# Performance work log

Hardware: AMD Instinct MI355X
Metric: run time of the kernel (lower is better)

Reference implementation:

```python
import jax, jax.numpy as jnp
import numpy as np

DIM = 768
HEADS = 12
DIM_HEAD = DIM // HEADS
FACTOR = DIM_HEAD ** (-0.5)
B, T = 4, 2048


def setup_inputs() -> dict:
    key = jax.random.key(0)
    k1, k2, k3 = jax.random.split(key, 3)
    x = jax.random.normal(k1, (B, T, DIM), dtype=jnp.float32)
    # VarianceScaling-like init scale for linear weights
    W_qkv = jax.random.normal(k2, (DIM, 3 * DIM), dtype=jnp.float32) * (DIM ** -0.5)
    W_out = jax.random.normal(k3, (DIM, DIM), dtype=jnp.float32) * (DIM ** -0.5)
    return {"x": x, "W_qkv": W_qkv, "W_out": W_out}


def reference(x, W_qkv, W_out):
    b, t, _ = x.shape
    qkv = x @ W_qkv  # [b, t, 3*dim]
    # einops 'b t (d k h) -> k b h t d' with k=3, h=HEADS: d slowest, k middle, h fastest
    qkv = qkv.reshape(b, t, DIM_HEAD, 3, HEADS)
    qkv = jnp.transpose(qkv, (3, 0, 4, 1, 2))  # [3, b, h, t, d]
    q, k, v = qkv[0], qkv[1], qkv[2]
    # scaled dot-product attention, full [b,h,t,t] scores as in the original
    scores = jnp.einsum('bhid,bhjd->bhij', q, k) * FACTOR
    attn = jax.nn.softmax(scores, axis=-1)
    out = jnp.einsum('bhij,bhjd->bhid', attn, v)  # [b, h, t, d]
    # 'b h t d -> b t (h d)'
    out = jnp.transpose(out, (0, 2, 1, 3)).reshape(b, t, HEADS * DIM_HEAD)
    return out @ W_out
```

## Files before the change

### kernel.cpp

```cpp
#include <hip/hip_runtime.h>
#include <hip/hip_bf16.h>

#define DIM    768
#define HEADS  12
#define DHEAD  64
#define BATCH  4
#define SEQ    2048
#define NROW   (BATCH * SEQ)
#define QKVN   (3 * DIM)
#define FACTOR 0.125f
#define QSCALE 0.18033688011112042f

typedef __attribute__((ext_vector_type(8))) short short8;
typedef __attribute__((ext_vector_type(4))) float floatx4;

__device__ __forceinline__ floatx4 mfma16(short8 a, short8 b, floatx4 c) {
    return __builtin_amdgcn_mfma_f32_16x16x32_bf16(a, b, c, 0, 0, 0);
}

__device__ __forceinline__ void glds16(const void* g, void* l) {
    __builtin_amdgcn_global_load_lds((const __attribute__((address_space(1))) void*)g,
                                     (__attribute__((address_space(3))) void*)l,
                                     16, 0, 0);
}

__device__ __forceinline__ short rne16(float f) {
    unsigned u = __builtin_bit_cast(unsigned, f);
    return (short)((u + 0x7fffu + ((u >> 16) & 1u)) >> 16);
}
__device__ __forceinline__ unsigned pack2(float lo, float hi) {
    unsigned ul = __builtin_bit_cast(unsigned, lo);
    unsigned uh = __builtin_bit_cast(unsigned, hi);
    ul = (ul + 0x7fffu + ((ul >> 16) & 1u)) >> 16;
    uh = (uh + 0x7fffu + ((uh >> 16) & 1u)) & 0xffff0000u;
    return ul | uh;
}
__device__ __forceinline__ unsigned cvtpk(float lo, float hi) {
    unsigned r;
    asm("v_cvt_pk_bf16_f32 %0, %1, %2" : "=v"(r) : "v"(lo), "v"(hi));
    return r;
}

__device__ __forceinline__ int swz8(int row, int col) {
    return (row << 6) + ((((col >> 3) ^ row) & 7) << 3) + (col & 7);
}

__global__ __launch_bounds__(256) void prep(const float* __restrict__ x,
                                            short* __restrict__ xb,
                                            const float* __restrict__ Wqkv,
                                            short* __restrict__ Wqt,
                                            const float* __restrict__ Wout,
                                            short* __restrict__ Wot) {
    __shared__ short T[32][33];
    int blk = blockIdx.x;
    if (blk < 6144) {
        int g = blk * 256 + threadIdx.x;
        float4 v = ((const float4*)x)[g];
        uint2 o;
        o.x = pack2(v.x, v.y);
        o.y = pack2(v.z, v.w);
        ((uint2*)xb)[g] = o;
        return;
    }
    blk -= 6144;
    const float* W;
    short* Wt;
    int N, permute, bx, by;
    if (blk < 1728) { W = Wqkv; Wt = Wqt; N = QKVN; permute = 1; bx = blk % 72; by = blk / 72; }
    else { blk -= 1728; W = Wout; Wt = Wot; N = DIM; permute = 0; bx = blk % 24; by = blk / 24; }

    int n0 = bx * 32, k0 = by * 32;
    int c = threadIdx.x & 31, r0 = threadIdx.x >> 5;
    for (int r = r0; r < 32; r += 8)
        T[r][c] = rne16(W[(size_t)(k0 + r) * N + n0 + c]);
    __syncthreads();
    for (int r = r0; r < 32; r += 8) {
        int n = n0 + r;
        int np = n;
        float scale = 1.0f;
        if (permute) {
            int d = n / 36, rem = n - d * 36;
            int which = rem / 12, h = rem - which * 12;
            np = which * 768 + h * 64 + d;
            if (which == 0) scale = QSCALE;
        }
        float v = __bfloat162float(__hip_bfloat16_raw{(unsigned short)T[c][r]});
        Wt[(size_t)np * DIM + k0 + c] = (scale == 1.0f) ? T[c][r] : rne16(v * scale);
    }
}

__global__ __launch_bounds__(256) void gemm_qkv(const short* __restrict__ A,
                                                const short* __restrict__ Bt,
                                                short* __restrict__ Qo,
                                                short* __restrict__ Ko,
                                                short* __restrict__ Vto) {
    __shared__ short As[128 * 64];
    __shared__ short Bs[128 * 64];
    const int tid = threadIdx.x;
    const int lane = tid & 63, wave = tid >> 6;
    const int l15 = lane & 15, quad = lane >> 4;

    const int flat = blockIdx.x;
    const int xcd = flat & 7;
    const int local = flat >> 3;
    const int mloc = local & 7, nloc = local >> 3;
    const int m0 = (xcd * 8 + mloc) * 128;
    const int n0 = nloc * 128;

    const int wm = (wave >> 1) * 64, wn = (wave & 1) * 64;
    const int r8 = wave * 8 + (lane >> 3);
    const int c8 = lane & 7;
    const int sc = ((c8 ^ (r8 & 7)) << 3);

    const int sn = n0 + wn;
    const int which = sn / 768;
    const bool swapAB = (which != 2);

    floatx4 acc[4][4] = {};
    for (int k0 = 0; k0 < DIM; k0 += 64) {
#pragma unroll
        for (int i = 0; i < 4; ++i) {
            int row = i * 32 + r8;
            glds16(&A[(size_t)(m0 + row) * DIM + k0 + sc], &As[(size_t)(i * 32 + wave * 8) * 64]);
            glds16(&Bt[(size_t)(n0 + row) * DIM + k0 + sc], &Bs[(size_t)(i * 32 + wave * 8) * 64]);
        }
        __syncthreads();
#pragma unroll
        for (int ks = 0; ks < 2; ++ks) {
            short8 a[4], b[4];
#pragma unroll
            for (int mt = 0; mt < 4; ++mt)
                a[mt] = *(const short8*)&As[swz8(wm + mt * 16 + l15, ks * 32 + quad * 8)];
#pragma unroll
            for (int nt = 0; nt < 4; ++nt)
                b[nt] = *(const short8*)&Bs[swz8(wn + nt * 16 + l15, ks * 32 + quad * 8)];
            if (swapAB) {
#pragma unroll
                for (int mt = 0; mt < 4; ++mt)
#pragma unroll
                    for (int nt = 0; nt < 4; ++nt)
                        acc[mt][nt] = mfma16(b[nt], a[mt], acc[mt][nt]);
            } else {
#pragma unroll
                for (int mt = 0; mt < 4; ++mt)
#pragma unroll
                    for (int nt = 0; nt < 4; ++nt)
                        acc[mt][nt] = mfma16(a[mt], b[nt], acc[mt][nt]);
            }
        }
        __syncthreads();
    }

    const int h = (sn - which * 768) >> 6;
    const int bb = (m0 + wm) >> 11;
    const int tbase = (m0 + wm) & 2047;
    const size_t tilebase = ((size_t)(bb * HEADS + h) * 32 + (tbase >> 6)) * 4096;

    if (which != 2) {
        short* dst = (which == 0) ? Qo : Ko;
#pragma unroll
        for (int mt = 0; mt < 4; ++mt)
#pragma unroll
            for (int nt = 0; nt < 4; ++nt) {
                int tl = mt * 16 + l15;
                int d0 = nt * 16 + quad * 4;
                uint2 pk;
                pk.x = pack2(acc[mt][nt][0], acc[mt][nt][1]);
                pk.y = pack2(acc[mt][nt][2], acc[mt][nt][3]);
                *(uint2*)&dst[tilebase + swz8(tl, d0)] = pk;
            }
    } else {
        short* vld = ((wave < 2) ? As : Bs) + (wave & 1) * 4096;
#pragma unroll
        for (int mt = 0; mt < 4; ++mt)
#pragma unroll
            for (int nt = 0; nt < 4; ++nt) {
                int d = nt * 16 + l15;
                int tl = mt * 16 + quad * 4;
                int chunk = (tl >> 3) ^ (d & 7);
                int addr = (d << 6) + (chunk << 3) + (tl & 7);
                uint2 pk;
                pk.x = pack2(acc[mt][nt][0], acc[mt][nt][1]);
                pk.y = pack2(acc[mt][nt][2], acc[mt][nt][3]);
                *(uint2*)&vld[addr] = pk;
            }
    }
    __syncthreads();
    if (which == 2) {
        short* vld = ((wave < 2) ? As : Bs) + (wave & 1) * 4096;
#pragma unroll
        for (int i = 0; i < 8; ++i) {
            int c = (i * 64 + lane) * 8;
            *(uint4*)&Vto[tilebase + c] = *(const uint4*)&vld[c];
        }
    }
}

__global__ __launch_bounds__(512, 6) void attn_mfma(const short* __restrict__ Q,
                                                    const short* __restrict__ K,
                                                    const short* __restrict__ Vt,
                                                    short* __restrict__ O) {
    __shared__ __align__(16) short smem[24576];
    const int tid = threadIdx.x;
    const int lane = tid & 63, wave = tid >> 6;
    const int l15 = lane & 15, quad = lane >> 4;
    const int flat = blockIdx.x;
    const int xcd = flat & 7, li = flat >> 3;
    const int bh = xcd + (li % 6) * 8;
    const int q0 = (li / 6) * 128;
    const size_t base = (size_t)bh * SEQ * DHEAD;
    short* Pp = smem + 16384 + wave * 1024;
    const int lane8 = lane * 8;

    {
        size_t qtb = base + (size_t)(q0 >> 6) * 4096;
#pragma unroll
        for (int c = 0; c < 2; ++c) {
            int i = wave * 2 + c;
            glds16(&Q[qtb + (size_t)i * 512 + lane8], &smem[i * 512]);
        }
    }
    __syncthreads();
    short8 qf[2];
#pragma unroll
    for (int ks = 0; ks < 2; ++ks)
        qf[ks] = *(const short8*)&smem[(wave >> 2) * 4096 +
                                       swz8((wave & 3) * 16 + l15,
                                            ks * 32 + quad * 8)];
    __syncthreads();

    floatx4 o[4] = {};
    float lsum = 0.f;

    glds16(&K[base + wave * 512 + lane8], &smem[wave * 512]);
    glds16(&Vt[base + wave * 512 + lane8], &smem[4096 + wave * 512]);

    for (int t = 0; t < 32; ++t) {
        __syncthreads();
        short* Ks = smem + (t & 1) * 8192;
        short* Vs = Ks + 4096;
        if (t < 31) {
            size_t ktb = base + (size_t)(t + 1) * 4096;
            short* nb = smem + ((t + 1) & 1) * 8192;
            glds16(&K[ktb + wave * 512 + lane8], &nb[wave * 512]);
            glds16(&Vt[ktb + wave * 512 + lane8], &nb[4096 + wave * 512]);
        }

        floatx4 sa[4] = {};
        __builtin_amdgcn_s_setprio(1);
#pragma unroll
        for (int ks = 0; ks < 2; ++ks)
#pragma unroll
            for (int kt = 0; kt < 4; ++kt) {
                short8 kf = *(const short8*)&Ks[swz8(kt * 16 + l15, ks * 32 + quad * 8)];
                sa[kt] = mfma16(kf, qf[ks], sa[kt]);
            }
        __builtin_amdgcn_s_setprio(0);

#pragma unroll
        for (int kt = 0; kt < 4; ++kt) {
            float p0 = __builtin_amdgcn_exp2f(sa[kt][0]);
            float p1 = __builtin_amdgcn_exp2f(sa[kt][1]);
            float p2 = __builtin_amdgcn_exp2f(sa[kt][2]);
            float p3 = __builtin_amdgcn_exp2f(sa[kt][3]);
            lsum += (p0 + p1) + (p2 + p3);
            uint2 pk;
            pk.x = cvtpk(p0, p1);
            pk.y = cvtpk(p2, p3);
            *(uint2*)&Pp[swz8(l15, kt * 16 + quad * 4)] = pk;
        }

#pragma unroll
        for (int ks = 0; ks < 2; ++ks) {
            short8 pf = *(const short8*)&Pp[swz8(l15, ks * 32 + quad * 8)];
            __builtin_amdgcn_s_setprio(1);
#pragma unroll
            for (int dt = 0; dt < 4; ++dt) {
                short8 vf = *(const short8*)&Vs[swz8(dt * 16 + l15, ks * 32 + quad * 8)];
                o[dt] = mfma16(vf, pf, o[dt]);
            }
            __builtin_amdgcn_s_setprio(0);
        }
    }

    float s = lsum;
    s += __shfl_xor(s, 16);
    s += __shfl_xor(s, 32);
    float inv = 1.f / s;

    const int b = bh / HEADS, h = bh - b * HEADS;
    const int tq = q0 + wave * 16 + l15;
    size_t rowo = ((size_t)(b * SEQ + tq)) * DIM + h * DHEAD + quad * 4;
#pragma unroll
    for (int dt = 0; dt < 4; ++dt) {
        uint2 pk;
        pk.x = cvtpk(o[dt][0] * inv, o[dt][1] * inv);
        pk.y = cvtpk(o[dt][2] * inv, o[dt][3] * inv);
        *(uint2*)&O[rowo + dt * 16] = pk;
    }
}

__global__ __launch_bounds__(256) void gemm_out(const short* __restrict__ A,
                                                const short* __restrict__ Bt,
                                                float* __restrict__ out) {
    __shared__ short As[128 * 64];
    __shared__ short Bs[128 * 64];
    const int tid = threadIdx.x;
    const int lane = tid & 63, wave = tid >> 6;
    const int l15 = lane & 15, quad = lane >> 4;
    const int m0 = blockIdx.y * 128, n0 = blockIdx.x * 128;
    const int wm = (wave >> 1) * 64, wn = (wave & 1) * 64;
    const int r8 = wave * 8 + (lane >> 3);
    const int sc = (((lane & 7) ^ (r8 & 7)) << 3);

    floatx4 acc[4][4] = {};
    for (int k0 = 0; k0 < DIM; k0 += 64) {
#pragma unroll
        for (int i = 0; i < 4; ++i) {
            int row = i * 32 + r8;
            glds16(&A[(size_t)(m0 + row) * DIM + k0 + sc], &As[(size_t)(i * 32 + wave * 8) * 64]);
            glds16(&Bt[(size_t)(n0 + row) * DIM + k0 + sc], &Bs[(size_t)(i * 32 + wave * 8) * 64]);
        }
        __syncthreads();
#pragma unroll
        for (int ks = 0; ks < 2; ++ks) {
            short8 a[4], b[4];
#pragma unroll
            for (int mt = 0; mt < 4; ++mt)
                a[mt] = *(const short8*)&As[swz8(wm + mt * 16 + l15, ks * 32 + quad * 8)];
#pragma unroll
            for (int nt = 0; nt < 4; ++nt)
                b[nt] = *(const short8*)&Bs[swz8(wn + nt * 16 + l15, ks * 32 + quad * 8)];
#pragma unroll
            for (int mt = 0; mt < 4; ++mt)
#pragma unroll
                for (int nt = 0; nt < 4; ++nt)
                    acc[mt][nt] = mfma16(b[nt], a[mt], acc[mt][nt]);
        }
        __syncthreads();
    }

#pragma unroll
    for (int mt = 0; mt < 4; ++mt)
#pragma unroll
        for (int nt = 0; nt < 4; ++nt) {
            int m = m0 + wm + mt * 16 + l15;
            int n = n0 + wn + nt * 16 + quad * 4;
            *(floatx4*)&out[(size_t)m * DIM + n] = acc[mt][nt];
        }
}

extern "C" void kernel_launch(void* const* d_in, const int* in_sizes, int n_in,
                              void* d_out, int out_size, void* d_ws, size_t ws_size,
                              hipStream_t stream) {
    const float* x    = (const float*)d_in[0];
    const float* Wqkv = (const float*)d_in[1];
    const float* Wout = (const float*)d_in[2];
    float* out = (float*)d_out;

    const size_t NE = (size_t)NROW * DIM;
    short* xb  = (short*)d_ws;
    short* Wqt = xb + NE;
    short* Wot = Wqt + (size_t)QKVN * DIM;
    short* Qw  = Wot + (size_t)DIM * DIM;
    short* Kw  = Qw + NE;
    short* Vtw = Kw + NE;

    prep<<<6144 + 1728 + 576, 256, 0, stream>>>(x, xb, Wqkv, Wqt, Wout, Wot);
    gemm_qkv<<<8 * 8 * 18, 256, 0, stream>>>(xb, Wqt, Qw, Kw, Vtw);
    attn_mfma<<<768, 512, 0, stream>>>(Qw, Kw, Vtw, xb);
    gemm_out<<<dim3(DIM / 128, NROW / 128), 256, 0, stream>>>(xb, Wot, out);
}
```

Before: 210.1 us.

## Switch attention to 32x32x16 MFMA with register-only P via permlane swaps

Attention now uses 32x32x16 bf16 MFMA with 4 waves of 32 query rows each, instead of 8 waves of 16 rows using 16x16x32. The softmax probabilities are repacked into B-operand fragments in registers with v_permlane32_swap, which removes the LDS round-trip for P. The QKV GEMM epilogue writes Q, K and Vt directly in the fragment-native layout, dropping the LDS transpose and the extra barrier for V. This reduces LDS traffic and instruction count, at the cost of fewer waves per block and more registers per wave.

```diff
diff --git a/kernel.cpp b/kernel.cpp
--- a/kernel.cpp
+++ b/kernel.cpp
@@ -13,9 +13,14 @@
 
 typedef __attribute__((ext_vector_type(8))) short short8;
 typedef __attribute__((ext_vector_type(4))) float floatx4;
+typedef __attribute__((ext_vector_type(16))) float floatx16;
+typedef __attribute__((ext_vector_type(4))) unsigned uintx4;
 
 __device__ __forceinline__ floatx4 mfma16(short8 a, short8 b, floatx4 c) {
     return __builtin_amdgcn_mfma_f32_16x16x32_bf16(a, b, c, 0, 0, 0);
+}
+__device__ __forceinline__ floatx16 mfma32(short8 a, short8 b, floatx16 c) {
+    return __builtin_amdgcn_mfma_f32_32x32x16_bf16(a, b, c, 0, 0, 0);
 }
 
 __device__ __forceinline__ void glds16(const void* g, void* l) {
@@ -153,150 +158,168 @@
 
     const int h = (sn - which * 768) >> 6;
     const int bb = (m0 + wm) >> 11;
-    const int tbase = (m0 + wm) & 2047;
-    const size_t tilebase = ((size_t)(bb * HEADS + h) * 32 + (tbase >> 6)) * 4096;
 
     if (which != 2) {
-        short* dst = (which == 0) ? Qo : Ko;
+        const bool isQ = (which == 0);
+        short* dst = isQ ? Qo : Ko;
+        const size_t tb = isQ
+            ? ((size_t)(bb * HEADS + h) * 16 + ((m0 & 2047) >> 7)) * 8192
+            : ((size_t)(bb * HEADS + h) * 32 + (((m0 + wm) & 2047) >> 6)) * 4096;
 #pragma unroll
         for (int mt = 0; mt < 4; ++mt)
 #pragma unroll
             for (int nt = 0; nt < 4; ++nt) {
-                int tl = mt * 16 + l15;
-                int d0 = nt * 16 + quad * 4;
+                int cl = (mt & 1) * 16 + l15 + 32 * (quad >> 1);
+                int off = isQ
+                    ? (((wm >> 5) + (mt >> 1)) * 2048 + nt * 512 + cl * 8 + (quad & 1) * 4)
+                    : (((mt >> 1) * 4 + nt) * 512 + cl * 8 + (quad & 1) * 4);
                 uint2 pk;
                 pk.x = pack2(acc[mt][nt][0], acc[mt][nt][1]);
                 pk.y = pack2(acc[mt][nt][2], acc[mt][nt][3]);
-                *(uint2*)&dst[tilebase + swz8(tl, d0)] = pk;
+                *(uint2*)&dst[tb + off] = pk;
             }
     } else {
-        short* vld = ((wave < 2) ? As : Bs) + (wave & 1) * 4096;
+        const size_t tb = ((size_t)(bb * HEADS + h) * 32 + (((m0 + wm) & 2047) >> 6)) * 4096;
 #pragma unroll
         for (int mt = 0; mt < 4; ++mt)
 #pragma unroll
             for (int nt = 0; nt < 4; ++nt) {
-                int d = nt * 16 + l15;
-                int tl = mt * 16 + quad * 4;
-                int chunk = (tl >> 3) ^ (d & 7);
-                int addr = (d << 6) + (chunk << 3) + (tl & 7);
+                int cl = (nt & 1) * 16 + l15 + 32 * (quad >> 1);
+                int off = ((nt >> 1) * 4 + mt) * 512 + cl * 8 + (quad & 1) * 4;
                 uint2 pk;
                 pk.x = pack2(acc[mt][nt][0], acc[mt][nt][1]);
                 pk.y = pack2(acc[mt][nt][2], acc[mt][nt][3]);
-                *(uint2*)&vld[addr] = pk;
+                *(uint2*)&Vto[tb + off] = pk;
             }
     }
-    __syncthreads();
-    if (which == 2) {
-        short* vld = ((wave < 2) ? As : Bs) + (wave & 1) * 4096;
-#pragma unroll
-        for (int i = 0; i < 8; ++i) {
-            int c = (i * 64 + lane) * 8;
-            *(uint4*)&Vto[tilebase + c] = *(const uint4*)&vld[c];
-        }
-    }
-}
-
-__global__ __launch_bounds__(512, 6) void attn_mfma(const short* __restrict__ Q,
+}
+
+__global__ __launch_bounds__(256, 3) void attn_mfma(const short* __restrict__ Q,
                                                     const short* __restrict__ K,
                                                     const short* __restrict__ Vt,
                                                     short* __restrict__ O) {
-    __shared__ __align__(16) short smem[24576];
+    __shared__ __align__(16) short smem[16384];
     const int tid = threadIdx.x;
     const int lane = tid & 63, wave = tid >> 6;
-    const int l15 = lane & 15, quad = lane >> 4;
+    const int l31 = lane & 31, hi = lane >> 5;
     const int flat = blockIdx.x;
     const int xcd = flat & 7, li = flat >> 3;
     const int bh = xcd + (li % 6) * 8;
     const int q0 = (li / 6) * 128;
     const size_t base = (size_t)bh * SEQ * DHEAD;
-    short* Pp = smem + 16384 + wave * 1024;
     const int lane8 = lane * 8;
 
     {
-        size_t qtb = base + (size_t)(q0 >> 6) * 4096;
-#pragma unroll
-        for (int c = 0; c < 2; ++c) {
-            int i = wave * 2 + c;
-            glds16(&Q[qtb + (size_t)i * 512 + lane8], &smem[i * 512]);
+        size_t qtb = base + (size_t)(q0 >> 7) * 8192;
+#pragma unroll
+        for (int c = 0; c < 4; ++c) {
+            int s = wave * 4 + c;
+            glds16(&Q[qtb + s * 512 + lane8], &smem[s * 512]);
         }
     }
     __syncthreads();
-    short8 qf[2];
-#pragma unroll
-    for (int ks = 0; ks < 2; ++ks)
-        qf[ks] = *(const short8*)&smem[(wave >> 2) * 4096 +
-                                       swz8((wave & 3) * 16 + l15,
-                                            ks * 32 + quad * 8)];
+    short8 qf[4];
+#pragma unroll
+    for (int ks = 0; ks < 4; ++ks)
+        qf[ks] = *(const short8*)&smem[wave * 2048 + ks * 512 + lane8];
     __syncthreads();
 
-    floatx4 o[4] = {};
+    floatx16 o0 = {}, o1 = {};
     float lsum = 0.f;
 
-    glds16(&K[base + wave * 512 + lane8], &smem[wave * 512]);
-    glds16(&Vt[base + wave * 512 + lane8], &smem[4096 + wave * 512]);
+    glds16(&K[base + (2 * wave + 0) * 512 + lane8], &smem[(2 * wave + 0) * 512]);
+    glds16(&K[base + (2 * wave + 1) * 512 + lane8], &smem[(2 * wave + 1) * 512]);
+    glds16(&Vt[base + (2 * wave + 0) * 512 + lane8], &smem[4096 + (2 * wave + 0) * 512]);
+    glds16(&Vt[base + (2 * wave + 1) * 512 + lane8], &smem[4096 + (2 * wave + 1) * 512]);
 
     for (int t = 0; t < 32; ++t) {
         __syncthreads();
-        short* Ks = smem + (t & 1) * 8192;
-        short* Vs = Ks + 4096;
+        const short* Ks = smem + (t & 1) * 8192;
+        const short* Vs = Ks + 4096;
         if (t < 31) {
             size_t ktb = base + (size_t)(t + 1) * 4096;
             short* nb = smem + ((t + 1) & 1) * 8192;
-            glds16(&K[ktb + wave * 512 + lane8], &nb[wave * 512]);
-            glds16(&Vt[ktb + wave * 512 + lane8], &nb[4096 + wave * 512]);
-        }
-
-        floatx4 sa[4] = {};
+            glds16(&K[ktb + (2 * wave + 0) * 512 + lane8], &nb[(2 * wave + 0) * 512]);
+            glds16(&K[ktb + (2 * wave + 1) * 512 + lane8], &nb[(2 * wave + 1) * 512]);
+            glds16(&Vt[ktb + (2 * wave + 0) * 512 + lane8], &nb[4096 + (2 * wave + 0) * 512]);
+            glds16(&Vt[ktb + (2 * wave + 1) * 512 + lane8], &nb[4096 + (2 * wave + 1) * 512]);
+        }
+
+        floatx16 sa0 = {}, sa1 = {};
         __builtin_amdgcn_s_setprio(1);
 #pragma unroll
-        for (int ks = 0; ks < 2; ++ks)
-#pragma unroll
-            for (int kt = 0; kt < 4; ++kt) {
-                short8 kf = *(const short8*)&Ks[swz8(kt * 16 + l15, ks * 32 + quad * 8)];
-                sa[kt] = mfma16(kf, qf[ks], sa[kt]);
-            }
+        for (int ks = 0; ks < 4; ++ks) {
+            short8 kf0 = *(const short8*)&Ks[(0 * 4 + ks) * 512 + lane8];
+            short8 kf1 = *(const short8*)&Ks[(1 * 4 + ks) * 512 + lane8];
+            sa0 = mfma32(kf0, qf[ks], sa0);
+            sa1 = mfma32(kf1, qf[ks], sa1);
+        }
         __builtin_amdgcn_s_setprio(0);
 
-#pragma unroll
-        for (int kt = 0; kt < 4; ++kt) {
-            float p0 = __builtin_amdgcn_exp2f(sa[kt][0]);
-            float p1 = __builtin_amdgcn_exp2f(sa[kt][1]);
-            float p2 = __builtin_amdgcn_exp2f(sa[kt][2]);
-            float p3 = __builtin_amdgcn_exp2f(sa[kt][3]);
-            lsum += (p0 + p1) + (p2 + p3);
-            uint2 pk;
-            pk.x = cvtpk(p0, p1);
-            pk.y = cvtpk(p2, p3);
-            *(uint2*)&Pp[swz8(l15, kt * 16 + quad * 4)] = pk;
-        }
-
-#pragma unroll
-        for (int ks = 0; ks < 2; ++ks) {
-            short8 pf = *(const short8*)&Pp[swz8(l15, ks * 32 + quad * 8)];
-            __builtin_amdgcn_s_setprio(1);
-#pragma unroll
-            for (int dt = 0; dt < 4; ++dt) {
-                short8 vf = *(const short8*)&Vs[swz8(dt * 16 + l15, ks * 32 + quad * 8)];
-                o[dt] = mfma16(vf, pf, o[dt]);
-            }
-            __builtin_amdgcn_s_setprio(0);
-        }
-    }
-
-    float s = lsum;
-    s += __shfl_xor(s, 16);
-    s += __shfl_xor(s, 32);
+        short8 pf[4];
+#define SOFTPACK(SA, PFA, PFB) {                                              \
+        float e0_  = __builtin_amdgcn_exp2f(SA[0]);                           \
+        float e1_  = __builtin_amdgcn_exp2f(SA[1]);                           \
+        float e2_  = __builtin_amdgcn_exp2f(SA[2]);                           \
+        float e3_  = __builtin_amdgcn_exp2f(SA[3]);                           \
+        float e4_  = __builtin_amdgcn_exp2f(SA[4]);                           \
+        float e5_  = __builtin_amdgcn_exp2f(SA[5]);                           \
+        float e6_  = __builtin_amdgcn_exp2f(SA[6]);                           \
+        float e7_  = __builtin_amdgcn_exp2f(SA[7]);                           \
+        float e8_  = __builtin_amdgcn_exp2f(SA[8]);                           \
+        float e9_  = __builtin_amdgcn_exp2f(SA[9]);                           \
+        float e10_ = __builtin_amdgcn_exp2f(SA[10]);                          \
+        float e11_ = __builtin_amdgcn_exp2f(SA[11]);                          \
+        float e12_ = __builtin_amdgcn_exp2f(SA[12]);                          \
+        float e13_ = __builtin_amdgcn_exp2f(SA[13]);                          \
+        float e14_ = __builtin_amdgcn_exp2f(SA[14]);                          \
+        float e15_ = __builtin_amdgcn_exp2f(SA[15]);                          \
+        lsum += (((e0_ + e1_) + (e2_ + e3_)) + ((e4_ + e5_) + (e6_ + e7_)))   \
+              + (((e8_ + e9_) + (e10_ + e11_)) + ((e12_ + e13_) + (e14_ + e15_))); \
+        unsigned A0_ = cvtpk(e0_, e1_),   A1_ = cvtpk(e2_, e3_);              \
+        unsigned B0_ = cvtpk(e4_, e5_),   B1_ = cvtpk(e6_, e7_);              \
+        unsigned C0_ = cvtpk(e8_, e9_),   C1_ = cvtpk(e10_, e11_);            \
+        unsigned E0_ = cvtpk(e12_, e13_), E1_ = cvtpk(e14_, e15_);            \
+        asm("v_permlane32_swap_b32 %0, %1" : "+v"(A0_), "+v"(B0_));           \
+        asm("v_permlane32_swap_b32 %0, %1" : "+v"(A1_), "+v"(B1_));           \
+        asm("v_permlane32_swap_b32 %0, %1" : "+v"(C0_), "+v"(E0_));           \
+        asm("v_permlane32_swap_b32 %0, %1" : "+v"(C1_), "+v"(E1_));           \
+        uintx4 wa_ = {A0_, A1_, B0_, B1_};                                    \
+        uintx4 wb_ = {C0_, C1_, E0_, E1_};                                    \
+        PFA = __builtin_bit_cast(short8, wa_);                                \
+        PFB = __builtin_bit_cast(short8, wb_);                                \
+    }
+        SOFTPACK(sa0, pf[0], pf[1])
+        SOFTPACK(sa1, pf[2], pf[3])
+#undef SOFTPACK
+
+        __builtin_amdgcn_s_setprio(1);
+#pragma unroll
+        for (int kc = 0; kc < 4; ++kc) {
+            short8 vf0 = *(const short8*)&Vs[(0 * 4 + kc) * 512 + lane8];
+            short8 vf1 = *(const short8*)&Vs[(1 * 4 + kc) * 512 + lane8];
+            o0 = mfma32(vf0, pf[kc], o0);
+            o1 = mfma32(vf1, pf[kc], o1);
+        }
+        __builtin_amdgcn_s_setprio(0);
+    }
+
+    float s = lsum + __shfl_xor(lsum, 32);
     float inv = 1.f / s;
 
     const int b = bh / HEADS, h = bh - b * HEADS;
-    const int tq = q0 + wave * 16 + l15;
-    size_t rowo = ((size_t)(b * SEQ + tq)) * DIM + h * DHEAD + quad * 4;
-#pragma unroll
-    for (int dt = 0; dt < 4; ++dt) {
-        uint2 pk;
-        pk.x = cvtpk(o[dt][0] * inv, o[dt][1] * inv);
-        pk.y = cvtpk(o[dt][2] * inv, o[dt][3] * inv);
-        *(uint2*)&O[rowo + dt * 16] = pk;
+    const int tq = q0 + wave * 32 + l31;
+    size_t rowo = ((size_t)(b * SEQ + tq)) * DIM + h * DHEAD;
+#pragma unroll
+    for (int blk = 0; blk < 4; ++blk) {
+        int d0 = 8 * blk + 4 * hi;
+        uint2 p0, p1;
+        p0.x = cvtpk(o0[4 * blk + 0] * inv, o0[4 * blk + 1] * inv);
+        p0.y = cvtpk(o0[4 * blk + 2] * inv, o0[4 * blk + 3] * inv);
+        *(uint2*)&O[rowo + d0] = p0;
+        p1.x = cvtpk(o1[4 * blk + 0] * inv, o1[4 * blk + 1] * inv);
+        p1.y = cvtpk(o1[4 * blk + 2] * inv, o1[4 * blk + 3] * inv);
+        *(uint2*)&O[rowo + 32 + d0] = p1;
     }
 }
 
@@ -368,6 +391,6 @@
 
     prep<<<6144 + 1728 + 576, 256, 0, stream>>>(x, xb, Wqkv, Wqt, Wout, Wot);
     gemm_qkv<<<8 * 8 * 18, 256, 0, stream>>>(xb, Wqt, Qw, Kw, Vtw);
-    attn_mfma<<<768, 512, 0, stream>>>(Qw, Kw, Vtw, xb);
+    attn_mfma<<<768, 256, 0, stream>>>(Qw, Kw, Vtw, xb);
     gemm_out<<<dim3(DIM / 128, NROW / 128), 256, 0, stream>>>(xb, Wot, out);
 }
```

After: 210.1 us. About the same (-0.0%).
